# Kernel optimization log

Hardware: AMD Instinct MI355X
Metric: run time of the kernel (lower is better)

The kernel has to match this reference:

```python
import jax, jax.numpy as jnp
import numpy as np
from jax import lax

KEEP_PROB = 0.9
BLOCK_SIZE = 7


def setup_inputs() -> dict:
    key = jax.random.key(0)
    x = jax.random.normal(key, (64, 64, 112, 112), dtype=jnp.float32)
    return {"x": x}


def _block_mask(init_mask, k):
    # Faithful vectorized form of the nested-loop dilation:
    # original zeroes out[i-k : i+k, j-k : j+k) (exclusive upper bound) around
    # every zero in init_mask, i.e. out[a,b] = min over i in [a-k+1, a+k],
    # j in [b-k+1, b+k] of init_mask -> min-pool (erosion) with window 2k,
    # asymmetric padding (k-1, k). Padding with init value 1.0 is the identity
    # for min on a {0,1} mask.
    return lax.reduce_window(
        init_mask,
        jnp.array(1.0, init_mask.dtype),
        lax.min,
        window_dimensions=(1, 2 * k, 2 * k),
        window_strides=(1, 1, 1),
        padding=((0, 0), (k - 1, k), (k - 1, k)),
    )


def reference(x):
    B, C, H, W = x.shape
    bs = BLOCK_SIZE
    # gamma = (1-keep_prob) * H^2 / (bs^2 * (H-bs+1)^2)
    gamma = (1.0 - KEEP_PROB) * (H ** 2) / (bs ** 2 * (H - bs + 1) ** 2)
    key = jax.random.key(42)
    # bernoulli(1-gamma): 1 = keep, 0 = drop-center
    init_mask = jax.random.bernoulli(key, 1.0 - gamma, (B, H, W)).astype(x.dtype)
    mask = _block_mask(init_mask, bs // 2)  # [B, H, W]
    out = x * mask[:, None, :, :]
    # renormalize: * (B*H*W) / sum(out)  (matches original, sums over all elems)
    out = out * (B * H * W) / jnp.sum(out)
    return out
```

## Files before the change

kernel.cpp:

```cpp
#include <hip/hip_runtime.h>
#include <stdint.h>

#define B_      64
#define C_      64
#define H_      112
#define W_      112
#define HW_     12544
#define NMASK_  802816
#define CHW_    802816
#define NTOT_   51380224
#define NV4_    12845056

__device__ __forceinline__ uint32_t rotl32(uint32_t x, int d) {
  return (x << d) | (x >> (32 - d));
}

__device__ __forceinline__ uint32_t threefry_bits(uint32_t i) {
  const uint32_t k0 = 0u, k1 = 42u;
  const uint32_t k2 = k0 ^ k1 ^ 0x1BD11BDAu;
  uint32_t x0 = 0u, x1 = i;
  x0 += k0; x1 += k1;
#define TF_R(r) { x0 += x1; x1 = rotl32(x1, (r)); x1 ^= x0; }
  TF_R(13) TF_R(15) TF_R(26) TF_R(6)
  x0 += k1; x1 += k2 + 1u;
  TF_R(17) TF_R(29) TF_R(16) TF_R(24)
  x0 += k2; x1 += k0 + 2u;
  TF_R(13) TF_R(15) TF_R(26) TF_R(6)
  x0 += k0; x1 += k1 + 3u;
  TF_R(17) TF_R(29) TF_R(16) TF_R(24)
  x0 += k1; x1 += k2 + 4u;
  TF_R(13) TF_R(15) TF_R(26) TF_R(6)
  x0 += k2; x1 += k0 + 5u;
#undef TF_R
  return x0 ^ x1;
}

__global__ void k_init_mask(uint8_t* __restrict__ init,
                            double* __restrict__ sum, float p) {
  int i = blockIdx.x * blockDim.x + threadIdx.x;
  if (i == 0) *sum = 0.0;
  if (i >= NMASK_) return;
  uint32_t bits = threefry_bits((uint32_t)i);
  float u = __uint_as_float((bits >> 9) | 0x3f800000u) - 1.0f;
  init[i] = (u < p) ? (uint8_t)1 : (uint8_t)0;
}

__global__ void k_erode_rows(const uint8_t* __restrict__ init,
                             uint8_t* __restrict__ tmp) {
  int t = blockIdx.x * blockDim.x + threadIdx.x;
  if (t >= NMASK_) return;
  int b = t / HW_;
  int rem = t - b * HW_;
  int a = rem / W_;
  int j = rem - a * W_;
  int lo = a - 2; if (lo < 0) lo = 0;
  int hi = a + 3; if (hi > H_ - 1) hi = H_ - 1;
  const uint8_t* base = init + b * HW_ + j;
  unsigned v = 1u;
  for (int i = lo; i <= hi; ++i) v &= base[i * W_];
  tmp[t] = (uint8_t)v;
}

__global__ void k_erode_cols(const uint8_t* __restrict__ tmp,
                             uint8_t* __restrict__ mask) {
  int t = blockIdx.x * blockDim.x + threadIdx.x;
  if (t >= NMASK_) return;
  int b = t / HW_;
  int rem = t - b * HW_;
  int a = rem / W_;
  int j = rem - a * W_;
  int lo = j - 2; if (lo < 0) lo = 0;
  int hi = j + 3; if (hi > W_ - 1) hi = W_ - 1;
  const uint8_t* row = tmp + b * HW_ + a * W_;
  unsigned v = 1u;
  for (int jj = lo; jj <= hi; ++jj) v &= row[jj];
  mask[t] = (uint8_t)v;
}

__global__ void k_sum(const float4* __restrict__ x4,
                      const uint8_t* __restrict__ mask,
                      double* __restrict__ sum) {
  float acc = 0.0f;
  int stride = gridDim.x * blockDim.x;
  for (int f = blockIdx.x * blockDim.x + threadIdx.x; f < NV4_; f += stride) {
    float4 v = x4[f];
    int e = f << 2;
    int b = e / CHW_;
    int hw = (e - b * CHW_) % HW_;
    uint32_t mw = *(const uint32_t*)(mask + b * HW_ + hw);
    acc += (mw & 0x000000ffu) ? v.x : 0.0f;
    acc += (mw & 0x0000ff00u) ? v.y : 0.0f;
    acc += (mw & 0x00ff0000u) ? v.z : 0.0f;
    acc += (mw & 0xff000000u) ? v.w : 0.0f;
  }
  for (int off = 32; off > 0; off >>= 1)
    acc += __shfl_down(acc, off, 64);
  __shared__ float part[4];
  int lane = threadIdx.x & 63;
  int wv = threadIdx.x >> 6;
  if (lane == 0) part[wv] = acc;
  __syncthreads();
  if (threadIdx.x == 0)
    atomicAdd(sum, (double)(part[0] + part[1] + part[2] + part[3]));
}

__global__ void k_scale(const float4* __restrict__ x4,
                        const uint8_t* __restrict__ mask,
                        const double* __restrict__ sum,
                        float4* __restrict__ out4) {
  float s = (float)(*sum);
  float scale = 802816.0f / s;
  int stride = gridDim.x * blockDim.x;
  for (int f = blockIdx.x * blockDim.x + threadIdx.x; f < NV4_; f += stride) {
    float4 v = x4[f];
    int e = f << 2;
    int b = e / CHW_;
    int hw = (e - b * CHW_) % HW_;
    uint32_t mw = *(const uint32_t*)(mask + b * HW_ + hw);
    float4 o;
    o.x = (mw & 0x000000ffu) ? v.x * scale : 0.0f;
    o.y = (mw & 0x0000ff00u) ? v.y * scale : 0.0f;
    o.z = (mw & 0x00ff0000u) ? v.z * scale : 0.0f;
    o.w = (mw & 0xff000000u) ? v.w * scale : 0.0f;
    out4[f] = o;
  }
}

extern "C" void kernel_launch(void* const* d_in, const int* in_sizes, int n_in,
                              void* d_out, int out_size, void* d_ws, size_t ws_size,
                              hipStream_t stream) {
  const float* x = (const float*)d_in[0];
  float* out = (float*)d_out;
  char* ws = (char*)d_ws;
  double* sum = (double*)ws;
  uint8_t* mA = (uint8_t*)(ws + 16);
  uint8_t* mB = mA + NMASK_;

  double gamma = (1.0 - 0.9) * 12544.0 / 550564.0;
  float p = (float)(1.0 - gamma);

  int mblk = (NMASK_ + 255) / 256;
  k_init_mask<<<mblk, 256, 0, stream>>>(mA, sum, p);
  k_erode_rows<<<mblk, 256, 0, stream>>>(mA, mB);
  k_erode_cols<<<mblk, 256, 0, stream>>>(mB, mA);
  k_sum<<<2048, 256, 0, stream>>>((const float4*)x, mA, sum);
  k_scale<<<8192, 256, 0, stream>>>((const float4*)x, mA, sum, (float4*)out);
}
```

Before: 398.3 us.

## Fuse mask generation and erosion in LDS, replace atomic sum with partials

The three mask kernels (RNG, row erosion, column erosion) become one kernel with one 1024-thread block per batch image, keeping intermediates in shared memory. The double atomicAdd reduction is replaced by per-block partials plus a single-block finalize kernel that computes the scale once. The output store in the scale kernel now uses a nontemporal store. This cuts launches and global traffic for the mask, but the mask kernel runs only 64 blocks, which may underuse the GPU.

```diff
diff --git a/kernel.cpp b/kernel.cpp
--- a/kernel.cpp
+++ b/kernel.cpp
@@ -2,14 +2,14 @@
 #include <stdint.h>
 
 #define B_      64
-#define C_      64
 #define H_      112
 #define W_      112
 #define HW_     12544
-#define NMASK_  802816
 #define CHW_    802816
-#define NTOT_   51380224
 #define NV4_    12845056
+#define NSUMBLK 2048
+
+typedef float v4f __attribute__((ext_vector_type(4)));
 
 __device__ __forceinline__ uint32_t rotl32(uint32_t x, int d) {
   return (x << d) | (x >> (32 - d));
@@ -35,54 +35,43 @@
   return x0 ^ x1;
 }
 
-__global__ void k_init_mask(uint8_t* __restrict__ init,
-                            double* __restrict__ sum, float p) {
-  int i = blockIdx.x * blockDim.x + threadIdx.x;
-  if (i == 0) *sum = 0.0;
-  if (i >= NMASK_) return;
-  uint32_t bits = threefry_bits((uint32_t)i);
-  float u = __uint_as_float((bits >> 9) | 0x3f800000u) - 1.0f;
-  init[i] = (u < p) ? (uint8_t)1 : (uint8_t)0;
+__global__ __launch_bounds__(1024) void k_mask(uint8_t* __restrict__ mask,
+                                               float p) {
+  __shared__ uint8_t t0[HW_];
+  __shared__ uint8_t t1[HW_];
+  const int b = blockIdx.x;
+  const int tid = threadIdx.x;
+  for (int c = tid; c < HW_; c += 1024) {
+    uint32_t bits = threefry_bits((uint32_t)(b * HW_ + c));
+    float u = __uint_as_float((bits >> 9) | 0x3f800000u) - 1.0f;
+    t0[c] = (u < p) ? (uint8_t)1 : (uint8_t)0;
+  }
+  __syncthreads();
+  for (int c = tid; c < HW_; c += 1024) {
+    int a = c / W_, j = c - a * W_;
+    int lo = a - 2; if (lo < 0) lo = 0;
+    int hi = a + 3; if (hi > H_ - 1) hi = H_ - 1;
+    unsigned v = 1u;
+    for (int i = lo; i <= hi; ++i) v &= t0[i * W_ + j];
+    t1[c] = (uint8_t)v;
+  }
+  __syncthreads();
+  for (int c = tid; c < HW_; c += 1024) {
+    int a = c / W_, j = c - a * W_;
+    int lo = j - 2; if (lo < 0) lo = 0;
+    int hi = j + 3; if (hi > W_ - 1) hi = W_ - 1;
+    unsigned v = 1u;
+    for (int jj = lo; jj <= hi; ++jj) v &= t1[a * W_ + jj];
+    mask[b * HW_ + c] = (uint8_t)v;
+  }
 }
 
-__global__ void k_erode_rows(const uint8_t* __restrict__ init,
-                             uint8_t* __restrict__ tmp) {
-  int t = blockIdx.x * blockDim.x + threadIdx.x;
-  if (t >= NMASK_) return;
-  int b = t / HW_;
-  int rem = t - b * HW_;
-  int a = rem / W_;
-  int j = rem - a * W_;
-  int lo = a - 2; if (lo < 0) lo = 0;
-  int hi = a + 3; if (hi > H_ - 1) hi = H_ - 1;
-  const uint8_t* base = init + b * HW_ + j;
-  unsigned v = 1u;
-  for (int i = lo; i <= hi; ++i) v &= base[i * W_];
-  tmp[t] = (uint8_t)v;
-}
-
-__global__ void k_erode_cols(const uint8_t* __restrict__ tmp,
-                             uint8_t* __restrict__ mask) {
-  int t = blockIdx.x * blockDim.x + threadIdx.x;
-  if (t >= NMASK_) return;
-  int b = t / HW_;
-  int rem = t - b * HW_;
-  int a = rem / W_;
-  int j = rem - a * W_;
-  int lo = j - 2; if (lo < 0) lo = 0;
-  int hi = j + 3; if (hi > W_ - 1) hi = W_ - 1;
-  const uint8_t* row = tmp + b * HW_ + a * W_;
-  unsigned v = 1u;
-  for (int jj = lo; jj <= hi; ++jj) v &= row[jj];
-  mask[t] = (uint8_t)v;
-}
-
-__global__ void k_sum(const float4* __restrict__ x4,
-                      const uint8_t* __restrict__ mask,
-                      double* __restrict__ sum) {
+__global__ __launch_bounds__(256) void k_sum(const float4* __restrict__ x4,
+                                             const uint8_t* __restrict__ mask,
+                                             float* __restrict__ partials) {
   float acc = 0.0f;
-  int stride = gridDim.x * blockDim.x;
-  for (int f = blockIdx.x * blockDim.x + threadIdx.x; f < NV4_; f += stride) {
+  const int stride = NSUMBLK * 256;
+  for (int f = blockIdx.x * 256 + threadIdx.x; f < NV4_; f += stride) {
     float4 v = x4[f];
     int e = f << 2;
     int b = e / CHW_;
@@ -96,33 +85,46 @@
   for (int off = 32; off > 0; off >>= 1)
     acc += __shfl_down(acc, off, 64);
   __shared__ float part[4];
-  int lane = threadIdx.x & 63;
-  int wv = threadIdx.x >> 6;
-  if (lane == 0) part[wv] = acc;
+  if ((threadIdx.x & 63) == 0) part[threadIdx.x >> 6] = acc;
   __syncthreads();
   if (threadIdx.x == 0)
-    atomicAdd(sum, (double)(part[0] + part[1] + part[2] + part[3]));
+    partials[blockIdx.x] = part[0] + part[1] + part[2] + part[3];
 }
 
-__global__ void k_scale(const float4* __restrict__ x4,
-                        const uint8_t* __restrict__ mask,
-                        const double* __restrict__ sum,
-                        float4* __restrict__ out4) {
-  float s = (float)(*sum);
-  float scale = 802816.0f / s;
-  int stride = gridDim.x * blockDim.x;
-  for (int f = blockIdx.x * blockDim.x + threadIdx.x; f < NV4_; f += stride) {
+__global__ __launch_bounds__(256) void k_fin(const float* __restrict__ partials,
+                                             float* __restrict__ scale) {
+  double acc = 0.0;
+  for (int i = threadIdx.x; i < NSUMBLK; i += 256)
+    acc += (double)partials[i];
+  for (int off = 32; off > 0; off >>= 1)
+    acc += __shfl_down(acc, off, 64);
+  __shared__ double part[4];
+  if ((threadIdx.x & 63) == 0) part[threadIdx.x >> 6] = acc;
+  __syncthreads();
+  if (threadIdx.x == 0) {
+    double s = part[0] + part[1] + part[2] + part[3];
+    *scale = (float)(802816.0 / s);
+  }
+}
+
+__global__ __launch_bounds__(256) void k_scale(const float4* __restrict__ x4,
+                                               const uint8_t* __restrict__ mask,
+                                               const float* __restrict__ scalep,
+                                               v4f* __restrict__ out4) {
+  const float scale = *scalep;
+  const int stride = gridDim.x * 256;
+  for (int f = blockIdx.x * 256 + threadIdx.x; f < NV4_; f += stride) {
     float4 v = x4[f];
     int e = f << 2;
     int b = e / CHW_;
     int hw = (e - b * CHW_) % HW_;
     uint32_t mw = *(const uint32_t*)(mask + b * HW_ + hw);
-    float4 o;
+    v4f o;
     o.x = (mw & 0x000000ffu) ? v.x * scale : 0.0f;
     o.y = (mw & 0x0000ff00u) ? v.y * scale : 0.0f;
     o.z = (mw & 0x00ff0000u) ? v.z * scale : 0.0f;
     o.w = (mw & 0xff000000u) ? v.w * scale : 0.0f;
-    out4[f] = o;
+    __builtin_nontemporal_store(o, &out4[f]);
   }
 }
 
@@ -132,17 +134,16 @@
   const float* x = (const float*)d_in[0];
   float* out = (float*)d_out;
   char* ws = (char*)d_ws;
-  double* sum = (double*)ws;
-  uint8_t* mA = (uint8_t*)(ws + 16);
-  uint8_t* mB = mA + NMASK_;
+  float* scale = (float*)ws;
+  float* partials = (float*)(ws + 16);
+  uint8_t* mask = (uint8_t*)(ws + 16384);
 
   double gamma = (1.0 - 0.9) * 12544.0 / 550564.0;
   float p = (float)(1.0 - gamma);
 
-  int mblk = (NMASK_ + 255) / 256;
-  k_init_mask<<<mblk, 256, 0, stream>>>(mA, sum, p);
-  k_erode_rows<<<mblk, 256, 0, stream>>>(mA, mB);
-  k_erode_cols<<<mblk, 256, 0, stream>>>(mB, mA);
-  k_sum<<<2048, 256, 0, stream>>>((const float4*)x, mA, sum);
-  k_scale<<<8192, 256, 0, stream>>>((const float4*)x, mA, sum, (float4*)out);
+  k_mask <<<B_,      1024, 0, stream>>>(mask, p);
+  k_sum  <<<NSUMBLK, 256,  0, stream>>>((const float4*)x, mask, partials);
+  k_fin  <<<1,       256,  0, stream>>>(partials, scale);
+  k_scale<<<8192,    256,  0, stream>>>((const float4*)x, mask, scale,
+                                        (v4f*)out);
 }
```

Measured after the change: 394.2 us. No clear change (-1.0%).
